# Kernel tuning notes

Measured on AMD Instinct MI355X. Metric: run time of the kernel, lower is better.

The kernel has to match this reference:

```python
import jax, jax.numpy as jnp
import numpy as np

B = 256          # number of images / sound groups
D = 512          # embedding dim
H = W = 16       # spatial dims of image feature map
SEG_LEN = 128    # avg sound tokens per sample
T = B * SEG_LEN  # total sound tokens


def setup_inputs() -> dict:
    key = jax.random.key(0)
    k1, k2 = jax.random.split(key)
    Z_img = jax.random.normal(k1, (B, D, H, W), dtype=jnp.float32)
    Z_snd = jax.random.normal(k2, (T, D), dtype=jnp.float32)
    # equal-length splits summing to T (torch.split lengths)
    snd_splits = jnp.full((B,), SEG_LEN, dtype=jnp.int64)
    return {"Z_img": Z_img, "Z_snd": Z_snd, "snd_splits": snd_splits}


def reference(Z_img, Z_snd, snd_splits):
    b, d = Z_img.shape[0], Z_img.shape[1]
    t = Z_snd.shape[0]
    # spatial mean pool: [B, D, H, W] -> [B, D]
    z_img = Z_img.reshape(b, d, -1).mean(axis=2)
    # ragged segment mean over variable splits (one fused pass, no Python loop)
    seg_ids = jnp.repeat(jnp.arange(b), snd_splits, total_repeat_length=t)
    seg_sum = jax.ops.segment_sum(Z_snd, seg_ids, num_segments=b)  # [B, D]
    z_snd = seg_sum / snd_splits[:, None].astype(Z_snd.dtype)
    # pairwise broadcast: [B_snd, B_img, D]
    M_img = jnp.broadcast_to(z_img[None, :, :], (b, b, d))
    M_snd = jnp.broadcast_to(z_snd[:, None, :], (b, b, d))
    return (M_img, M_snd)
```

## Files before the change

### kernel.cpp

```cpp
#include <hip/hip_runtime.h>

#define NB 256
#define ND 512
#define NHW 256
#define NSEG 128
#define NBD (NB * ND)
#define NREG ((size_t)NB * NB * ND)

__global__ __launch_bounds__(256) void pool_kernel(
    const float* __restrict__ img, const float* __restrict__ snd,
    float* __restrict__ zimg, float* __restrict__ zsnd)
{
    __shared__ float red[128][4];
    const int t = threadIdx.x;

    if (blockIdx.x < NB) {
        const int b    = blockIdx.x;
        const int cg   = t & 127;
        const int half = t >> 7;
        const float* base = snd + ((size_t)(b * NSEG + half * 64)) * ND + cg * 4;
        float a0 = 0.f, a1 = 0.f, a2 = 0.f, a3 = 0.f;
        #pragma unroll 8
        for (int r = 0; r < 64; ++r) {
            const float4 u = *(const float4*)(base + (size_t)r * ND);
            a0 += u.x; a1 += u.y; a2 += u.z; a3 += u.w;
        }
        if (half) { red[cg][0] = a0; red[cg][1] = a1; red[cg][2] = a2; red[cg][3] = a3; }
        __syncthreads();
        if (!half) {
            constexpr float s = 1.0f / NSEG;
            float4 o;
            o.x = (a0 + red[cg][0]) * s;
            o.y = (a1 + red[cg][1]) * s;
            o.z = (a2 + red[cg][2]) * s;
            o.w = (a3 + red[cg][3]) * s;
            *(float4*)(zsnd + b * ND + cg * 4) = o;
        }
    } else {
        const int lane = t & 63;
        const int wave = t >> 6;
        const int row0 = ((blockIdx.x - NB) * 4 + wave) * 4;
        const float* base = img + (size_t)row0 * NHW + lane * 4;
        float m[4];
        #pragma unroll
        for (int r = 0; r < 4; ++r) {
            const float4 u = *(const float4*)(base + (size_t)r * NHW);
            float s = u.x + u.y + u.z + u.w;
            #pragma unroll
            for (int msk = 32; msk; msk >>= 1) s += __shfl_xor(s, msk, 64);
            m[r] = s * (1.0f / NHW);
        }
        if (lane == 0) {
            float4 o; o.x = m[0]; o.y = m[1]; o.z = m[2]; o.w = m[3];
            *(float4*)(zimg + row0) = o;
        }
    }
}

__global__ __launch_bounds__(256) void bcast_kernel(
    const float4* __restrict__ zi, const float4* __restrict__ zs,
    float4* __restrict__ o)
{
    const size_t stride = (size_t)gridDim.x * 256;
    const size_t nvec = NREG * 2 / 4;
    for (size_t v = (size_t)blockIdx.x * 256 + threadIdx.x; v < nvec; v += stride) {
        const size_t k = v * 4;
        float4 val;
        if (k < NREG) {
            val = zi[(k & (size_t)(NBD - 1)) >> 2];
        } else {
            const size_t k2 = k - NREG;
            val = zs[((k2 >> 17) << 7) + ((k2 & 511) >> 2)];
        }
        o[v] = val;
    }
}

extern "C" void kernel_launch(void* const* d_in, const int* in_sizes, int n_in,
                              void* d_out, int out_size, void* d_ws, size_t ws_size,
                              hipStream_t stream) {
    const float* img = (const float*)d_in[0];
    const float* snd = (const float*)d_in[1];
    float* zimg = (float*)d_ws;
    float* zsnd = zimg + NBD;
    float* out  = (float*)d_out;

    pool_kernel<<<dim3(NB + 8192), dim3(256), 0, stream>>>(img, snd, zimg, zsnd);
    bcast_kernel<<<dim3(8192), dim3(256), 0, stream>>>(
        (const float4*)zimg, (const float4*)zsnd, (float4*)out);
}
```

Measured before the change: 403.2 us.

## Use nontemporal loads/stores and restructure pool and broadcast kernels

Pool reads now use nontemporal loads, and the image pooling is reorganised so each wave reduces 16 rows with 4 lanes per row and only a two-step shuffle, which needs a quarter of the blocks. The broadcast kernel drops the grid-stride loop with its per-element branch and index arithmetic. It now uses dedicated blocks: each sound block loads one vector once and writes it 32 times, and each image block copies a contiguous slab, all with nontemporal stores. The aim is to cut cache pollution and address math on a write-bound 268MB output, at the cost of a fixed-size grid that no longer generalises.

```diff
diff --git a/kernel.cpp b/kernel.cpp
--- a/kernel.cpp
+++ b/kernel.cpp
@@ -1,4 +1,6 @@
 #include <hip/hip_runtime.h>
+
+typedef float f4 __attribute__((ext_vector_type(4)));
 
 #define NB 256
 #define ND 512
@@ -6,6 +8,7 @@
 #define NSEG 128
 #define NBD (NB * ND)
 #define NREG ((size_t)NB * NB * ND)
+#define NREG4 (NREG / 4)
 
 __global__ __launch_bounds__(256) void pool_kernel(
     const float* __restrict__ img, const float* __restrict__ snd,
@@ -18,61 +21,62 @@
         const int b    = blockIdx.x;
         const int cg   = t & 127;
         const int half = t >> 7;
-        const float* base = snd + ((size_t)(b * NSEG + half * 64)) * ND + cg * 4;
+        const f4* base = (const f4*)(snd + ((size_t)(b * NSEG + half * 64)) * ND) + cg;
         float a0 = 0.f, a1 = 0.f, a2 = 0.f, a3 = 0.f;
         #pragma unroll 8
         for (int r = 0; r < 64; ++r) {
-            const float4 u = *(const float4*)(base + (size_t)r * ND);
+            const f4 u = __builtin_nontemporal_load(base + (size_t)r * (ND / 4));
             a0 += u.x; a1 += u.y; a2 += u.z; a3 += u.w;
         }
         if (half) { red[cg][0] = a0; red[cg][1] = a1; red[cg][2] = a2; red[cg][3] = a3; }
         __syncthreads();
         if (!half) {
             constexpr float s = 1.0f / NSEG;
-            float4 o;
+            f4 o;
             o.x = (a0 + red[cg][0]) * s;
             o.y = (a1 + red[cg][1]) * s;
             o.z = (a2 + red[cg][2]) * s;
             o.w = (a3 + red[cg][3]) * s;
-            *(float4*)(zsnd + b * ND + cg * 4) = o;
+            *((f4*)(zsnd + b * ND) + cg) = o;
         }
     } else {
         const int lane = t & 63;
         const int wave = t >> 6;
-        const int row0 = ((blockIdx.x - NB) * 4 + wave) * 4;
-        const float* base = img + (size_t)row0 * NHW + lane * 4;
-        float m[4];
+        const int r    = lane >> 2;
+        const int c    = lane & 3;
+        const int row  = (int)(blockIdx.x - NB) * 64 + wave * 16 + r;
+        const f4* base = (const f4*)(img + (size_t)row * NHW) + c;
+        f4 acc = {0.f, 0.f, 0.f, 0.f};
         #pragma unroll
-        for (int r = 0; r < 4; ++r) {
-            const float4 u = *(const float4*)(base + (size_t)r * NHW);
-            float s = u.x + u.y + u.z + u.w;
-            #pragma unroll
-            for (int msk = 32; msk; msk >>= 1) s += __shfl_xor(s, msk, 64);
-            m[r] = s * (1.0f / NHW);
-        }
-        if (lane == 0) {
-            float4 o; o.x = m[0]; o.y = m[1]; o.z = m[2]; o.w = m[3];
-            *(float4*)(zimg + row0) = o;
-        }
+        for (int i = 0; i < 16; ++i)
+            acc += __builtin_nontemporal_load(base + i * 4);
+        float s = acc.x + acc.y + acc.z + acc.w;
+        s += __shfl_xor(s, 1, 64);
+        s += __shfl_xor(s, 2, 64);
+        if (c == 0) zimg[row] = s * (1.0f / NHW);
     }
 }
 
 __global__ __launch_bounds__(256) void bcast_kernel(
-    const float4* __restrict__ zi, const float4* __restrict__ zs,
-    float4* __restrict__ o)
+    const f4* __restrict__ zi, const f4* __restrict__ zs,
+    f4* __restrict__ out)
 {
-    const size_t stride = (size_t)gridDim.x * 256;
-    const size_t nvec = NREG * 2 / 4;
-    for (size_t v = (size_t)blockIdx.x * 256 + threadIdx.x; v < nvec; v += stride) {
-        const size_t k = v * 4;
-        float4 val;
-        if (k < NREG) {
-            val = zi[(k & (size_t)(NBD - 1)) >> 2];
-        } else {
-            const size_t k2 = k - NREG;
-            val = zs[((k2 >> 17) << 7) + ((k2 & 511) >> 2)];
+    const int t = threadIdx.x;
+    if (blockIdx.x < 1024) {
+        const int i = blockIdx.x >> 2;
+        const int q = blockIdx.x & 3;
+        const f4 val = zs[i * 128 + (t & 127)];
+        f4* dst = out + NREG4 + (size_t)i * 32768 + q * 8192 + t;
+        #pragma unroll
+        for (int s = 0; s < 32; ++s)
+            __builtin_nontemporal_store(val, dst + s * 256);
+    } else {
+        const size_t base = (size_t)(blockIdx.x - 1024) * 2048;
+        #pragma unroll
+        for (int s = 0; s < 8; ++s) {
+            const size_t p = base + s * 256 + t;
+            __builtin_nontemporal_store(zi[p & 32767], out + p);
         }
-        o[v] = val;
     }
 }
 
@@ -83,9 +87,8 @@
     const float* snd = (const float*)d_in[1];
     float* zimg = (float*)d_ws;
     float* zsnd = zimg + NBD;
-    float* out  = (float*)d_out;
 
-    pool_kernel<<<dim3(NB + 8192), dim3(256), 0, stream>>>(img, snd, zimg, zsnd);
-    bcast_kernel<<<dim3(8192), dim3(256), 0, stream>>>(
-        (const float4*)zimg, (const float4*)zsnd, (float4*)out);
+    pool_kernel<<<dim3(NB + 2048), dim3(256), 0, stream>>>(img, snd, zimg, zsnd);
+    bcast_kernel<<<dim3(5120), dim3(256), 0, stream>>>(
+        (const f4*)zimg, (const f4*)zsnd, (f4*)d_out);
 }
```

Result: faster. 384.5 us (-4.6%).
